# Optimization experiments

Measured on AMD Instinct MI355X. Metric: run time of the kernel, lower is better.

Reference implementation:

```python
import jax, jax.numpy as jnp
import numpy as np

B, T, K, I, H = 64, 1024, 16, 3, 20  # batch, time, n_lstms, input, hidden


def setup_inputs() -> dict:
    key = jax.random.key(0)
    ks = jax.random.split(key, 8)
    s = 1.0 / np.sqrt(H)  # torch LSTM init scale
    inp = jax.random.normal(ks[0], (B, T, K, I), dtype=jnp.float32)
    w = jax.random.normal(ks[1], (K * B + 1,), dtype=jnp.float32)
    W_ih = jax.random.uniform(ks[2], (K, 4 * H, I), minval=-s, maxval=s, dtype=jnp.float32)
    W_hh = jax.random.uniform(ks[3], (K, 4 * H, H), minval=-s, maxval=s, dtype=jnp.float32)
    b_ih = jax.random.uniform(ks[4], (K, 4 * H), minval=-s, maxval=s, dtype=jnp.float32)
    b_hh = jax.random.uniform(ks[5], (K, 4 * H), minval=-s, maxval=s, dtype=jnp.float32)
    conv_w = jax.random.uniform(ks[6], (H + 1,), minval=-s, maxval=s, dtype=jnp.float32)
    conv_b = jax.random.uniform(ks[7], (), minval=-s, maxval=s, dtype=jnp.float32)
    return {"inp": inp, "w": w, "W_ih": W_ih, "W_hh": W_hh,
            "b_ih": b_ih, "b_hh": b_hh, "conv_w": conv_w, "conv_b": conv_b}


def _forward(inp, w, W_ih, W_hh, b_ih, b_hh, conv_w, conv_b):
    # Precompute input projections for all 16 LSTMs at once: [T, B, K, 4H]
    x_proj = jnp.einsum('btki,kgi->tbkg', inp, W_ih) + (b_ih + b_hh)

    def step(carry, xp):
        h, c = carry  # [B, K, H] each
        gates = xp + jnp.einsum('bkh,kgh->bkg', h, W_hh)
        i, f, g, o = jnp.split(gates, 4, axis=-1)  # torch gate order: i,f,g,o
        c = jax.nn.sigmoid(f) * c + jax.nn.sigmoid(i) * jnp.tanh(g)
        h = jax.nn.sigmoid(o) * jnp.tanh(c)
        return (h, c), None

    h0 = jnp.zeros((inp.shape[0], K, H), inp.dtype)
    (h, _), _ = jax.lax.scan(step, (h0, h0), x_proj)

    # torch cat order over dim=1: rnn0's batch, then rnn1's batch, ... => [K*B, H]
    hs = jnp.transpose(h, (1, 0, 2)).reshape(K * inp.shape[0], H)
    feat = jnp.concatenate([hs, w[1:][:, None]], axis=1)  # [K*B, 21]
    y = jnp.tanh(feat @ conv_w + conv_b)                  # pointwise Conv1d(21,1,1)
    y = jnp.concatenate([jnp.ones((1,), y.dtype), y])     # prepend constant 1 (cash)
    return jax.nn.softmax(y)


def reference(inp, w, W_ih, W_hh, b_ih, b_hh, conv_w, conv_b):
    return _forward(inp, w, W_ih, W_hh, b_ih, b_hh, conv_w, conv_b)
```

## Files before the change

kernel.cpp:

```cpp
#include <hip/hip_runtime.h>

#define TT 1024
#define KK 16
#define HH 20
#define NCELL 1024

typedef _Float16 f16;
typedef f16 f16x2 __attribute__((ext_vector_type(2)));

#define LOG2E 1.4426950408889634f

__device__ __forceinline__ float fdot2(f16x2 a, f16x2 b, float c) {
    return __builtin_amdgcn_fdot2(a, b, c, false);
}

__device__ __forceinline__ float fast_rcp(float x) {
    return __builtin_amdgcn_rcpf(x);
}

__device__ __forceinline__ float sigm2(float x2) {
    return fast_rcp(1.0f + __builtin_amdgcn_exp2f(-x2));
}

__device__ __forceinline__ float tanh_fast(float x) {
    float e = __builtin_amdgcn_exp2f(x * (2.0f * LOG2E));
    return 1.0f - 2.0f * fast_rcp(e + 1.0f);
}

__device__ __forceinline__ float bcast(float v, int srclane) {
    return __int_as_float(__builtin_amdgcn_readlane(__float_as_int(v), srclane));
}
__device__ __forceinline__ unsigned bcast_u(unsigned v, int srclane) {
    return (unsigned)__builtin_amdgcn_readlane((int)v, srclane);
}

__device__ __forceinline__ void half_bcast(float v, float& from_lo, float& from_hi) {
    float a = v, b = v;
    asm("v_permlane32_swap_b32 %0, %1" : "+v"(a), "+v"(b));
    from_lo = a; from_hi = b;
}

struct F3 { float x, y, z; };

__global__ __launch_bounds__(64)
__attribute__((amdgpu_waves_per_eu(1, 1)))
void lstm_kernel(
    const float* __restrict__ inp,
    const float* __restrict__ W_ih,
    const float* __restrict__ W_hh,
    const float* __restrict__ b_ih,
    const float* __restrict__ b_hh,
    const float* __restrict__ w,
    const float* __restrict__ conv_w,
    const float* __restrict__ conv_b,
    float* __restrict__ y_ws)
{
    const int lane = threadIdx.x;
    const int cell = blockIdx.x;
    const int k = cell >> 6;
    const int b = cell & 63;
    const int half = lane >> 5;
    const int jj = lane & 31;
    const int j = (jj < HH) ? jj : (HH - 1);

    f16x2 WpA[10], WpB[10];
    float WiA[3], WiB[3];
    float biasA, biasB;
    {
        const int rA = k * 80 + (half * 2) * HH + j;
        const int rB = rA + HH;
        const float scaleA = LOG2E * (half ? 2.0f : 1.0f);
        const float scaleB = LOG2E;
        #pragma unroll
        for (int m = 0; m < 10; ++m) {
            WpA[m] = f16x2{(f16)(W_hh[rA * HH + 2 * m] * scaleA),
                           (f16)(W_hh[rA * HH + 2 * m + 1] * scaleA)};
            WpB[m] = f16x2{(f16)(W_hh[rB * HH + 2 * m] * scaleB),
                           (f16)(W_hh[rB * HH + 2 * m + 1] * scaleB)};
        }
        #pragma unroll
        for (int i = 0; i < 3; ++i) {
            WiA[i] = W_ih[rA * 3 + i] * scaleA;
            WiB[i] = W_ih[rB * 3 + i] * scaleB;
        }
        biasA = (b_ih[rA] + b_hh[rA]) * scaleA;
        biasB = (b_ih[rB] + b_hh[rB]) * scaleB;
    }
    const float mA = half ? 2.0f : 1.0f;
    const float bA = half ? -1.0f : 0.0f;

    float h_own = 0.0f, c_own = 0.0f;

    const float* xb = inp + (b * TT * KK + k) * 3;
    F3 p0{xb[0 * 48], xb[0 * 48 + 1], xb[0 * 48 + 2]};
    F3 p1{xb[1 * 48], xb[1 * 48 + 1], xb[1 * 48 + 2]};
    F3 p2{xb[2 * 48], xb[2 * 48 + 1], xb[2 * 48 + 2]};
    F3 p3{xb[3 * 48], xb[3 * 48 + 1], xb[3 * 48 + 2]};

    auto step = [&](F3& p, int t) {
        unsigned hb = (unsigned)__builtin_bit_cast(unsigned short, (f16)h_own);
        unsigned nb = (unsigned)__builtin_amdgcn_mov_dpp((int)hb, 0xB1, 0xF, 0xF, true);
        const unsigned packed = hb | (nb << 16);
        f16x2 hp[10];
        #pragma unroll
        for (int m = 0; m < 10; ++m)
            hp[m] = __builtin_bit_cast(f16x2, bcast_u(packed, 2 * m));

        const float x0 = p.x, x1 = p.y, x2 = p.z;
        {
            int tn = t + 4; tn = (tn < TT) ? tn : (TT - 1);
            const float* q = xb + tn * (KK * 3);
            p.x = q[0]; p.y = q[1]; p.z = q[2];
        }
        const float eA = biasA + WiA[0] * x0 + WiA[1] * x1 + WiA[2] * x2;
        const float eB = biasB + WiB[0] * x0 + WiB[1] * x1 + WiB[2] * x2;
        float pA0 = eA, pA1 = 0.f, pB0 = eB, pB1 = 0.f;
        #pragma unroll
        for (int m = 0; m < 5; ++m) {
            pA0 = fdot2(WpA[m], hp[m], pA0);
            pB0 = fdot2(WpB[m], hp[m], pB0);
            pA1 = fdot2(WpA[m + 5], hp[m + 5], pA1);
            pB1 = fdot2(WpB[m + 5], hp[m + 5], pB1);
        }
        const float gA = pA0 + pA1;
        const float gB = pB0 + pB1;
        const float uA = sigm2(gA);
        const float actA = uA * mA + bA;
        const float actB = sigm2(gB);
        float sI, tG, sF, sO;
        half_bcast(actA, sI, tG);
        half_bcast(actB, sF, sO);
        c_own = sF * c_own + sI * tG;
        h_own = sO * tanh_fast(c_own);
    };

    for (int tb = 0; tb < TT; tb += 4) {
        step(p0, tb + 0);
        step(p1, tb + 1);
        step(p2, tb + 2);
        step(p3, tb + 3);
    }

    float acc = conv_b[0];
    #pragma unroll
    for (int hh = 0; hh < HH; ++hh) acc += conv_w[hh] * bcast(h_own, hh);
    acc += conv_w[HH] * w[1 + cell];
    if (lane == 0) y_ws[cell] = tanh_fast(acc);
}

__global__ __launch_bounds__(256) void softmax_kernel(
    const float* __restrict__ y_ws, float* __restrict__ out)
{
    __shared__ float red[4];
    const int tid = threadIdx.x;
    float vals[5];
    float local = 0.0f;
    #pragma unroll
    for (int it = 0; it < 5; ++it) {
        const int idx = tid + it * 256;
        if (idx < NCELL + 1) {
            const float y = (idx == 0) ? 1.0f : y_ws[idx - 1];
            const float e = __expf(y);
            vals[it] = e;
            local += e;
        } else {
            vals[it] = 0.0f;
        }
    }
    #pragma unroll
    for (int off = 32; off > 0; off >>= 1) local += __shfl_down(local, off, 64);
    if ((tid & 63) == 0) red[tid >> 6] = local;
    __syncthreads();
    const float total = red[0] + red[1] + red[2] + red[3];
    const float inv = 1.0f / total;
    #pragma unroll
    for (int it = 0; it < 5; ++it) {
        const int idx = tid + it * 256;
        if (idx < NCELL + 1) out[idx] = vals[it] * inv;
    }
}

extern "C" void kernel_launch(void* const* d_in, const int* in_sizes, int n_in,
                              void* d_out, int out_size, void* d_ws, size_t ws_size,
                              hipStream_t stream) {
    const float* inp    = (const float*)d_in[0];
    const float* w      = (const float*)d_in[1];
    const float* W_ih   = (const float*)d_in[2];
    const float* W_hh   = (const float*)d_in[3];
    const float* b_ih   = (const float*)d_in[4];
    const float* b_hh   = (const float*)d_in[5];
    const float* conv_w = (const float*)d_in[6];
    const float* conv_b = (const float*)d_in[7];
    float* out  = (float*)d_out;
    float* y_ws = (float*)d_ws;

    lstm_kernel<<<NCELL, 64, 0, stream>>>(inp, W_ih, W_hh, b_ih, b_hh, w,
                                          conv_w, conv_b, y_ws);
    softmax_kernel<<<1, 256, 0, stream>>>(y_ws, out);
}
```

Measured before the change: 185.3 us.

## Pack two LSTM cells per wave, each half-wave computing all four gates

Each 64-lane block now handles two cells, one per half-wave, with every lane computing all four gates for its hidden unit. This removes the permlane swap exchange and halves the number of blocks. The input projection and bias also move into fp16 dot2 instructions. In exchange each lane does twice the dot-product work per step, needs twice as many readlanes for the h broadcast, and the input and bias terms lose precision in fp16.

```diff
diff --git a/kernel.cpp b/kernel.cpp
--- a/kernel.cpp
+++ b/kernel.cpp
@@ -13,31 +13,21 @@
 __device__ __forceinline__ float fdot2(f16x2 a, f16x2 b, float c) {
     return __builtin_amdgcn_fdot2(a, b, c, false);
 }
-
 __device__ __forceinline__ float fast_rcp(float x) {
     return __builtin_amdgcn_rcpf(x);
 }
-
 __device__ __forceinline__ float sigm2(float x2) {
     return fast_rcp(1.0f + __builtin_amdgcn_exp2f(-x2));
 }
-
 __device__ __forceinline__ float tanh_fast(float x) {
     float e = __builtin_amdgcn_exp2f(x * (2.0f * LOG2E));
     return 1.0f - 2.0f * fast_rcp(e + 1.0f);
 }
-
 __device__ __forceinline__ float bcast(float v, int srclane) {
     return __int_as_float(__builtin_amdgcn_readlane(__float_as_int(v), srclane));
 }
 __device__ __forceinline__ unsigned bcast_u(unsigned v, int srclane) {
     return (unsigned)__builtin_amdgcn_readlane((int)v, srclane);
-}
-
-__device__ __forceinline__ void half_bcast(float v, float& from_lo, float& from_hi) {
-    float a = v, b = v;
-    asm("v_permlane32_swap_b32 %0, %1" : "+v"(a), "+v"(b));
-    from_lo = a; from_hi = b;
 }
 
 struct F3 { float x, y, z; };
@@ -55,39 +45,36 @@
     const float* __restrict__ conv_b,
     float* __restrict__ y_ws)
 {
-    const int lane = threadIdx.x;
-    const int cell = blockIdx.x;
-    const int k = cell >> 6;
-    const int b = cell & 63;
-    const int half = lane >> 5;
+    const int lane  = threadIdx.x;
+    const int bid   = blockIdx.x;
+    const int cellA = 2 * bid;
+    const int cellB = 2 * bid + 1;
+    const bool isA  = (lane < 32);
+    const int myCell = isA ? cellA : cellB;
+    const int k  = myCell >> 6;
+    const int b  = myCell & 63;
     const int jj = lane & 31;
-    const int j = (jj < HH) ? jj : (HH - 1);
-
-    f16x2 WpA[10], WpB[10];
-    float WiA[3], WiB[3];
-    float biasA, biasB;
+    const int j  = (jj < HH) ? jj : (HH - 1);
+
+    f16x2 Wh[4][10];
+    f16x2 Wx01[4];
+    f16x2 Wx2b[4];
     {
-        const int rA = k * 80 + (half * 2) * HH + j;
-        const int rB = rA + HH;
-        const float scaleA = LOG2E * (half ? 2.0f : 1.0f);
-        const float scaleB = LOG2E;
         #pragma unroll
-        for (int m = 0; m < 10; ++m) {
-            WpA[m] = f16x2{(f16)(W_hh[rA * HH + 2 * m] * scaleA),
-                           (f16)(W_hh[rA * HH + 2 * m + 1] * scaleA)};
-            WpB[m] = f16x2{(f16)(W_hh[rB * HH + 2 * m] * scaleB),
-                           (f16)(W_hh[rB * HH + 2 * m + 1] * scaleB)};
-        }
-        #pragma unroll
-        for (int i = 0; i < 3; ++i) {
-            WiA[i] = W_ih[rA * 3 + i] * scaleA;
-            WiB[i] = W_ih[rB * 3 + i] * scaleB;
-        }
-        biasA = (b_ih[rA] + b_hh[rA]) * scaleA;
-        biasB = (b_ih[rB] + b_hh[rB]) * scaleB;
-    }
-    const float mA = half ? 2.0f : 1.0f;
-    const float bA = half ? -1.0f : 0.0f;
+        for (int g = 0; g < 4; ++g) {
+            const int r = k * 80 + g * HH + j;
+            const float scale = LOG2E * ((g == 2) ? 2.0f : 1.0f);
+            #pragma unroll
+            for (int m = 0; m < 10; ++m) {
+                Wh[g][m] = f16x2{(f16)(W_hh[r * HH + 2 * m] * scale),
+                                 (f16)(W_hh[r * HH + 2 * m + 1] * scale)};
+            }
+            Wx01[g] = f16x2{(f16)(W_ih[r * 3 + 0] * scale),
+                            (f16)(W_ih[r * 3 + 1] * scale)};
+            Wx2b[g] = f16x2{(f16)(W_ih[r * 3 + 2] * scale),
+                            (f16)((b_ih[r] + b_hh[r]) * scale)};
+        }
+    }
 
     float h_own = 0.0f, c_own = 0.0f;
 
@@ -103,33 +90,42 @@
         const unsigned packed = hb | (nb << 16);
         f16x2 hp[10];
         #pragma unroll
-        for (int m = 0; m < 10; ++m)
-            hp[m] = __builtin_bit_cast(f16x2, bcast_u(packed, 2 * m));
-
+        for (int m = 0; m < 10; ++m) {
+            const unsigned pa = bcast_u(packed, 2 * m);
+            const unsigned pb = bcast_u(packed, 32 + 2 * m);
+            hp[m] = __builtin_bit_cast(f16x2, isA ? pa : pb);
+        }
         const float x0 = p.x, x1 = p.y, x2 = p.z;
         {
             int tn = t + 4; tn = (tn < TT) ? tn : (TT - 1);
             const float* q = xb + tn * (KK * 3);
             p.x = q[0]; p.y = q[1]; p.z = q[2];
         }
-        const float eA = biasA + WiA[0] * x0 + WiA[1] * x1 + WiA[2] * x2;
-        const float eB = biasB + WiB[0] * x0 + WiB[1] * x1 + WiB[2] * x2;
-        float pA0 = eA, pA1 = 0.f, pB0 = eB, pB1 = 0.f;
-        #pragma unroll
-        for (int m = 0; m < 5; ++m) {
-            pA0 = fdot2(WpA[m], hp[m], pA0);
-            pB0 = fdot2(WpB[m], hp[m], pB0);
-            pA1 = fdot2(WpA[m + 5], hp[m + 5], pA1);
-            pB1 = fdot2(WpB[m + 5], hp[m + 5], pB1);
-        }
-        const float gA = pA0 + pA1;
-        const float gB = pB0 + pB1;
-        const float uA = sigm2(gA);
-        const float actA = uA * mA + bA;
-        const float actB = sigm2(gB);
-        float sI, tG, sF, sO;
-        half_bcast(actA, sI, tG);
-        half_bcast(actB, sF, sO);
+        const f16x2 xp01 = f16x2{(f16)x0, (f16)x1};
+        const f16x2 xp2b = f16x2{(f16)x2, (f16)1.0f};
+        float a0, a1, a2, a3;
+        {
+            float q00 = fdot2(Wx01[0], xp01, fdot2(Wx2b[0], xp2b, 0.0f)), q01 = 0.f;
+            float q10 = fdot2(Wx01[1], xp01, fdot2(Wx2b[1], xp2b, 0.0f)), q11 = 0.f;
+            float q20 = fdot2(Wx01[2], xp01, fdot2(Wx2b[2], xp2b, 0.0f)), q21 = 0.f;
+            float q30 = fdot2(Wx01[3], xp01, fdot2(Wx2b[3], xp2b, 0.0f)), q31 = 0.f;
+            #pragma unroll
+            for (int m = 0; m < 5; ++m) {
+                q00 = fdot2(Wh[0][m], hp[m], q00);
+                q10 = fdot2(Wh[1][m], hp[m], q10);
+                q20 = fdot2(Wh[2][m], hp[m], q20);
+                q30 = fdot2(Wh[3][m], hp[m], q30);
+                q01 = fdot2(Wh[0][m + 5], hp[m + 5], q01);
+                q11 = fdot2(Wh[1][m + 5], hp[m + 5], q11);
+                q21 = fdot2(Wh[2][m + 5], hp[m + 5], q21);
+                q31 = fdot2(Wh[3][m + 5], hp[m + 5], q31);
+            }
+            a0 = q00 + q01; a1 = q10 + q11; a2 = q20 + q21; a3 = q30 + q31;
+        }
+        const float sI = sigm2(a0);
+        const float sF = sigm2(a1);
+        const float tG = sigm2(a2) * 2.0f - 1.0f;
+        const float sO = sigm2(a3);
         c_own = sF * c_own + sI * tG;
         h_own = sO * tanh_fast(c_own);
     };
@@ -141,11 +137,16 @@
         step(p3, tb + 3);
     }
 
-    float acc = conv_b[0];
-    #pragma unroll
-    for (int hh = 0; hh < HH; ++hh) acc += conv_w[hh] * bcast(h_own, hh);
-    acc += conv_w[HH] * w[1 + cell];
-    if (lane == 0) y_ws[cell] = tanh_fast(acc);
+    float accA = conv_b[0], accB = conv_b[0];
+    #pragma unroll
+    for (int hh = 0; hh < HH; ++hh) {
+        accA += conv_w[hh] * bcast(h_own, hh);
+        accB += conv_w[hh] * bcast(h_own, 32 + hh);
+    }
+    accA += conv_w[HH] * w[1 + cellA];
+    accB += conv_w[HH] * w[1 + cellB];
+    if (lane == 0) y_ws[cellA] = tanh_fast(accA);
+    if (lane == 1) y_ws[cellB] = tanh_fast(accB);
 }
 
 __global__ __launch_bounds__(256) void softmax_kernel(
@@ -194,7 +195,7 @@
     float* out  = (float*)d_out;
     float* y_ws = (float*)d_ws;
 
-    lstm_kernel<<<NCELL, 64, 0, stream>>>(inp, W_ih, W_hh, b_ih, b_hh, w,
-                                          conv_w, conv_b, y_ws);
+    lstm_kernel<<<NCELL / 2, 64, 0, stream>>>(inp, W_ih, W_hh, b_ih, b_hh, w,
+                                              conv_w, conv_b, y_ws);
     softmax_kernel<<<1, 256, 0, stream>>>(y_ws, out);
 }
```

After: 303.8 us. 63.9% more time.

## Stage LSTM inputs in LDS as packed fp16 and use fdot2 for input projection

Applied to the files above, without the earlier changes.

Before the recurrence, each block loads its whole input sequence into shared memory as packed fp16 (x0,x1,x2,1). Each step then reads one 8-byte LDS word instead of three strided global loads. The input projection and bias become two fdot2 ops per gate, with the bias folded in as an fp16 weight. This takes global-memory latency off the serial recurrence and cuts per-step scalar FMAs, at the cost of lower precision for inputs and bias and a prologue load with a sync.

```diff
diff --git a/kernel.cpp b/kernel.cpp
--- a/kernel.cpp
+++ b/kernel.cpp
@@ -13,20 +13,16 @@
 __device__ __forceinline__ float fdot2(f16x2 a, f16x2 b, float c) {
     return __builtin_amdgcn_fdot2(a, b, c, false);
 }
-
 __device__ __forceinline__ float fast_rcp(float x) {
     return __builtin_amdgcn_rcpf(x);
 }
-
 __device__ __forceinline__ float sigm2(float x2) {
     return fast_rcp(1.0f + __builtin_amdgcn_exp2f(-x2));
 }
-
 __device__ __forceinline__ float tanh_fast(float x) {
     float e = __builtin_amdgcn_exp2f(x * (2.0f * LOG2E));
     return 1.0f - 2.0f * fast_rcp(e + 1.0f);
 }
-
 __device__ __forceinline__ float bcast(float v, int srclane) {
     return __int_as_float(__builtin_amdgcn_readlane(__float_as_int(v), srclane));
 }
@@ -39,8 +35,6 @@
     asm("v_permlane32_swap_b32 %0, %1" : "+v"(a), "+v"(b));
     from_lo = a; from_hi = b;
 }
-
-struct F3 { float x, y, z; };
 
 __global__ __launch_bounds__(64)
 __attribute__((amdgpu_waves_per_eu(1, 1)))
@@ -55,6 +49,8 @@
     const float* __restrict__ conv_b,
     float* __restrict__ y_ws)
 {
+    __shared__ unsigned long long xs[TT];
+
     const int lane = threadIdx.x;
     const int cell = blockIdx.x;
     const int k = cell >> 6;
@@ -63,9 +59,19 @@
     const int jj = lane & 31;
     const int j = (jj < HH) ? jj : (HH - 1);
 
-    f16x2 WpA[10], WpB[10];
-    float WiA[3], WiB[3];
-    float biasA, biasB;
+    {
+        const float* xbg = inp + (b * TT * KK + k) * 3;
+        for (int t = lane; t < TT; t += 64) {
+            const float* q = xbg + t * (KK * 3);
+            const f16x2 lo = f16x2{(f16)q[0], (f16)q[1]};
+            const f16x2 hi = f16x2{(f16)q[2], (f16)1.0f};
+            xs[t] = ((unsigned long long)__builtin_bit_cast(unsigned, hi) << 32)
+                  | __builtin_bit_cast(unsigned, lo);
+        }
+    }
+
+    f16x2 WhA[10], WhB[10];
+    f16x2 WxA01, WxA2b, WxB01, WxB2b;
     {
         const int rA = k * 80 + (half * 2) * HH + j;
         const int rB = rA + HH;
@@ -73,31 +79,28 @@
         const float scaleB = LOG2E;
         #pragma unroll
         for (int m = 0; m < 10; ++m) {
-            WpA[m] = f16x2{(f16)(W_hh[rA * HH + 2 * m] * scaleA),
+            WhA[m] = f16x2{(f16)(W_hh[rA * HH + 2 * m] * scaleA),
                            (f16)(W_hh[rA * HH + 2 * m + 1] * scaleA)};
-            WpB[m] = f16x2{(f16)(W_hh[rB * HH + 2 * m] * scaleB),
+            WhB[m] = f16x2{(f16)(W_hh[rB * HH + 2 * m] * scaleB),
                            (f16)(W_hh[rB * HH + 2 * m + 1] * scaleB)};
         }
-        #pragma unroll
-        for (int i = 0; i < 3; ++i) {
-            WiA[i] = W_ih[rA * 3 + i] * scaleA;
-            WiB[i] = W_ih[rB * 3 + i] * scaleB;
-        }
-        biasA = (b_ih[rA] + b_hh[rA]) * scaleA;
-        biasB = (b_ih[rB] + b_hh[rB]) * scaleB;
+        WxA01 = f16x2{(f16)(W_ih[rA * 3 + 0] * scaleA), (f16)(W_ih[rA * 3 + 1] * scaleA)};
+        WxB01 = f16x2{(f16)(W_ih[rB * 3 + 0] * scaleB), (f16)(W_ih[rB * 3 + 1] * scaleB)};
+        WxA2b = f16x2{(f16)(W_ih[rA * 3 + 2] * scaleA),
+                      (f16)((b_ih[rA] + b_hh[rA]) * scaleA)};
+        WxB2b = f16x2{(f16)(W_ih[rB * 3 + 2] * scaleB),
+                      (f16)((b_ih[rB] + b_hh[rB]) * scaleB)};
     }
     const float mA = half ? 2.0f : 1.0f;
     const float bA = half ? -1.0f : 0.0f;
 
     float h_own = 0.0f, c_own = 0.0f;
 
-    const float* xb = inp + (b * TT * KK + k) * 3;
-    F3 p0{xb[0 * 48], xb[0 * 48 + 1], xb[0 * 48 + 2]};
-    F3 p1{xb[1 * 48], xb[1 * 48 + 1], xb[1 * 48 + 2]};
-    F3 p2{xb[2 * 48], xb[2 * 48 + 1], xb[2 * 48 + 2]};
-    F3 p3{xb[3 * 48], xb[3 * 48 + 1], xb[3 * 48 + 2]};
-
-    auto step = [&](F3& p, int t) {
+    __syncthreads();
+
+    unsigned long long xq0 = xs[0], xq1 = xs[1], xq2 = xs[2], xq3 = xs[3];
+
+    auto step = [&](unsigned long long& xq, int t) {
         unsigned hb = (unsigned)__builtin_bit_cast(unsigned short, (f16)h_own);
         unsigned nb = (unsigned)__builtin_amdgcn_mov_dpp((int)hb, 0xB1, 0xF, 0xF, true);
         const unsigned packed = hb | (nb << 16);
@@ -106,21 +109,21 @@
         for (int m = 0; m < 10; ++m)
             hp[m] = __builtin_bit_cast(f16x2, bcast_u(packed, 2 * m));
 
-        const float x0 = p.x, x1 = p.y, x2 = p.z;
+        const f16x2 xp01 = __builtin_bit_cast(f16x2, (unsigned)xq);
+        const f16x2 xp2b = __builtin_bit_cast(f16x2, (unsigned)(xq >> 32));
         {
             int tn = t + 4; tn = (tn < TT) ? tn : (TT - 1);
-            const float* q = xb + tn * (KK * 3);
-            p.x = q[0]; p.y = q[1]; p.z = q[2];
-        }
-        const float eA = biasA + WiA[0] * x0 + WiA[1] * x1 + WiA[2] * x2;
-        const float eB = biasB + WiB[0] * x0 + WiB[1] * x1 + WiB[2] * x2;
+            xq = xs[tn];
+        }
+        const float eA = fdot2(WxA01, xp01, fdot2(WxA2b, xp2b, 0.0f));
+        const float eB = fdot2(WxB01, xp01, fdot2(WxB2b, xp2b, 0.0f));
         float pA0 = eA, pA1 = 0.f, pB0 = eB, pB1 = 0.f;
         #pragma unroll
         for (int m = 0; m < 5; ++m) {
-            pA0 = fdot2(WpA[m], hp[m], pA0);
-            pB0 = fdot2(WpB[m], hp[m], pB0);
-            pA1 = fdot2(WpA[m + 5], hp[m + 5], pA1);
-            pB1 = fdot2(WpB[m + 5], hp[m + 5], pB1);
+            pA0 = fdot2(WhA[m], hp[m], pA0);
+            pB0 = fdot2(WhB[m], hp[m], pB0);
+            pA1 = fdot2(WhA[m + 5], hp[m + 5], pA1);
+            pB1 = fdot2(WhB[m + 5], hp[m + 5], pB1);
         }
         const float gA = pA0 + pA1;
         const float gB = pB0 + pB1;
@@ -135,10 +138,10 @@
     };
 
     for (int tb = 0; tb < TT; tb += 4) {
-        step(p0, tb + 0);
-        step(p1, tb + 1);
-        step(p2, tb + 2);
-        step(p3, tb + 3);
+        step(xq0, tb + 0);
+        step(xq1, tb + 1);
+        step(xq2, tb + 2);
+        step(xq3, tb + 3);
     }
 
     float acc = conv_b[0];
```

Result: faster. 162.2 us (-12.5%).
